# Kernel optimization log

Measured on AMD Instinct MI355X. Metric: run time of the kernel, lower is better.

The kernel has to match this reference:

```python
import jax, jax.numpy as jnp
import numpy as np

H, D, K, FF = 8, 512, 64, 64  # n_head, feature_dim, key_feature_dim, dim_feedforward
L, B = 512, 32
LN_EPS = 1e-5


def _l2norm(x, eps=1e-12):
    # torch F.normalize: x / max(||x||, eps)
    n = jnp.sqrt(jnp.sum(x * x, axis=-1, keepdims=True))
    return x / jnp.maximum(n, eps)


def _layernorm(x, g, b, eps=LN_EPS):
    m = jnp.mean(x, axis=-1, keepdims=True)
    v = jnp.mean((x - m) ** 2, axis=-1, keepdims=True)
    return (x - m) * jax.lax.rsqrt(v + eps) * g + b


def setup_inputs() -> dict:
    key0 = jax.random.key(0)
    ks = jax.random.split(key0, 13)
    n = jax.random.normal
    s_kq = float(np.sqrt(2.0 / K))
    s_v = float(np.sqrt(2.0 / D))
    return {
        "query": n(ks[0], (L, B, D), jnp.float32),
        "key": n(ks[1], (L, B, D), jnp.float32),
        "value": n(ks[2], (L, B, D), jnp.float32),
        "WK": n(ks[3], (H, K, D), jnp.float32) * s_kq,
        "WQ": n(ks[4], (H, K, D), jnp.float32) * s_kq,
        "WV": n(ks[5], (H, D, D), jnp.float32) * s_v,
        "Wt": n(ks[6], (H, D, D), jnp.float32) * 0.04,  # trans_conv (default kaiming-ish scale)
        "W1": n(ks[7], (H, FF, D), jnp.float32) * 0.04,
        "b1": jnp.zeros((H, FF), jnp.float32),
        "W2": n(ks[8], (H, D, FF), jnp.float32) * 0.1,
        "b2": jnp.zeros((H, D), jnp.float32),
        "ln_g": jnp.ones((H, D), jnp.float32),
        "ln_b": jnp.zeros((H, D), jnp.float32),
    }


def reference(query, key, value, WK, WQ, WV, Wt, W1, b1, W2, b2, ln_g, ln_b):
    # query/key/value: [L, B, D]; per-head weights stacked on leading H axis.
    Lq, Bb, Dd = query.shape
    Hh = WK.shape[0]

    # per-head cosine-normalized Q/K projections: [H, B, L, K]
    wq = _l2norm(jnp.einsum('lbd,hkd->hblk', query, WQ))
    wk = _l2norm(jnp.einsum('lbd,hkd->hblk', key, WK))

    # attention scores [H, B, Lq, Lk], temp = 1
    dot = jnp.einsum('hbqc,hbkc->hbqk', wq, wk)
    aff = jax.nn.softmax(dot, axis=-1)
    # custom renorm: divide by column sums over the QUERY axis
    aff = aff / (1e-9 + jnp.sum(aff, axis=2, keepdims=True))

    wv = jnp.einsum('lbd,hed->hble', value, WV)        # [H, B, Lk, D]
    out = jnp.einsum('hbqk,hbke->hbqe', aff, wv)       # [H, B, Lq, D]
    out = jnp.transpose(out, (0, 2, 1, 3))             # [H, L, B, D]

    # residual-style trans_conv(query - out) -> relu
    o = jax.nn.relu(jnp.einsum('hlbd,hed->hlbe', query[None] - out, Wt))

    # TransNonlinear FFN (dropout = identity at eval)
    hff = jax.nn.relu(jnp.einsum('hlbd,hfd->hlbf', o, W1) + b1[:, None, None, :])
    s2 = jnp.einsum('hlbf,hdf->hlbd', hff, W2) + b2[:, None, None, :]
    x = _layernorm(o + s2, ln_g[:, None, None, :], ln_b[:, None, None, :])

    # concat heads on last dim, head 0 first: [L, B, H*D]
    return jnp.transpose(x, (1, 2, 0, 3)).reshape(Lq, Bb, Hh * Dd)
```

## Files before the change

### kernel.cpp

```cpp
#include <hip/hip_runtime.h>
#include <stdint.h>

#define HH 8
#define DDIM 512
#define KHEAD 64
#define FFD 64
#define LLEN 512
#define BBATCH 32
#define NTOK 16384

typedef unsigned short u16;
typedef __attribute__((ext_vector_type(8))) __bf16 bf16x8;
typedef __attribute__((ext_vector_type(4))) float f32x4;

__device__ __forceinline__ float bf2f(u16 u) {
    union { uint32_t i; float f; } v; v.i = ((uint32_t)u) << 16; return v.f;
}
__device__ __forceinline__ u16 f2bf(float f) {
    union { uint32_t i; float f; } v; v.f = f;
    return (u16)((v.i + 0x7FFFu + ((v.i >> 16) & 1u)) >> 16);
}

__device__ __forceinline__ void gload16(const void* g, void* l) {
    __builtin_amdgcn_global_load_lds(
        (const __attribute__((address_space(1))) void*)g,
        (__attribute__((address_space(3))) void*)l, 16, 0, 0);
}

__global__ __launch_bounds__(256) void f2bf4(const float* __restrict__ in,
                                             u16* __restrict__ out, int n4) {
    int i = blockIdx.x * 256 + threadIdx.x;
    if (i >= n4) return;
    float4 v = ((const float4*)in)[i];
    ushort4 o; o.x = f2bf(v.x); o.y = f2bf(v.y); o.z = f2bf(v.z); o.w = f2bf(v.w);
    ((ushort4*)out)[i] = o;
}

enum { M_PLAIN = 0, M_WQK = 1, M_SUBAUX = 2, M_RELU = 3, M_ADDAUX = 4, M_SCALECOL = 5 };

template<int BM, int BN, int MODE>
__global__ __launch_bounds__(256) void mgemm(
    const u16* __restrict__ A, const u16* __restrict__ B, u16* __restrict__ C,
    int Kd, int lda, int ldb, int ldc,
    long Ash, long Asb, long Bsh, long Bsb, long Csh, long Csb, int nB2,
    const float* __restrict__ bias, int biasN,
    const void* __restrict__ auxp, long auxsh, long auxsb, int auxld)
{
    constexpr int WC = (BN == 128) ? 2 : 1;
    constexpr int WR = 4 / WC;
    constexpr int WTM = BM / WR;
    constexpr int WTN = BN / WC;
    constexpr int MF = WTM / 16;
    constexpr int NF = WTN / 16;
    constexpr int NCA = (BM * 64) / 4096;
    constexpr int NCB = (BN * 64) / 4096;
    __shared__ u16 As[BM * 32];
    __shared__ u16 Bs[BN * 32];

    const int z = blockIdx.z;
    const int h2 = z / nB2, b2 = z % nB2;
    const u16* Ab = A + h2 * Ash + b2 * Asb;
    const u16* Bb = B + h2 * Bsh + b2 * Bsb;
    const int m0 = blockIdx.x * BM, n0 = blockIdx.y * BN;
    const int t = threadIdx.x;
    const int lane = t & 63;
    const int w = t >> 6;
    const int wr = w / WC, wc = w % WC;
    const int tb = t * 16;
    const int wb = (t & 192) * 16;

    f32x4 acc[MF][NF];
    #pragma unroll
    for (int m = 0; m < MF; ++m)
        #pragma unroll
        for (int n = 0; n < NF; ++n)
            #pragma unroll
            for (int i = 0; i < 4; ++i) acc[m][n][i] = 0.f;

    const int ko = (lane >> 4) * 16;

    for (int k0 = 0; k0 < Kd; k0 += 32) {
        #pragma unroll
        for (int c = 0; c < NCA; ++c) {
            const int byte = c * 4096 + tb;
            const int row = byte >> 6;
            gload16((const char*)(Ab + (long)(m0 + row) * lda + k0) + (byte & 63),
                    (char*)As + c * 4096 + wb);
        }
        #pragma unroll
        for (int c = 0; c < NCB; ++c) {
            const int byte = c * 4096 + tb;
            const int row = byte >> 6;
            gload16((const char*)(Bb + (long)(n0 + row) * ldb + k0) + (byte & 63),
                    (char*)Bs + c * 4096 + wb);
        }
        __syncthreads();
        bf16x8 af[MF], bfr[NF];
        #pragma unroll
        for (int m = 0; m < MF; ++m)
            af[m] = *(const bf16x8*)((const char*)As + (wr * WTM + m * 16 + (lane & 15)) * 64 + ko);
        #pragma unroll
        for (int n = 0; n < NF; ++n)
            bfr[n] = *(const bf16x8*)((const char*)Bs + (wc * WTN + n * 16 + (lane & 15)) * 64 + ko);
        #pragma unroll
        for (int m = 0; m < MF; ++m)
            #pragma unroll
            for (int n = 0; n < NF; ++n)
                acc[m][n] = __builtin_amdgcn_mfma_f32_16x16x32_bf16(af[m], bfr[n], acc[m][n], 0, 0, 0);
        __syncthreads();
    }

    const int lr = (lane >> 4) * 4;
    const int lc = lane & 15;

    if constexpr (MODE == M_WQK) {
        const int h = (n0 + wc * WTN) >> 6;
        #pragma unroll
        for (int m = 0; m < MF; ++m) {
            #pragma unroll
            for (int i = 0; i < 4; ++i) {
                float s = 0.f;
                #pragma unroll
                for (int n = 0; n < NF; ++n) { const float v = acc[m][n][i]; s += v * v; }
                s += __shfl_xor(s, 1); s += __shfl_xor(s, 2);
                s += __shfl_xor(s, 4); s += __shfl_xor(s, 8);
                const float inv = 1.0f / fmaxf(sqrtf(s), 1e-12f);
                const int r = m0 + wr * WTM + m * 16 + lr + i;
                const int l = r >> 5, bq = r & 31;
                const int sw = (l & 7) << 3;
                u16* rowp = C + (((long)(h * BBATCH + bq) * LLEN + l) * KHEAD);
                #pragma unroll
                for (int n = 0; n < NF; ++n)
                    rowp[(lc + n * 16) ^ sw] = f2bf(acc[m][n][i] * inv);
            }
        }
    } else {
        const long cof = h2 * Csh + b2 * Csb;
        #pragma unroll
        for (int m = 0; m < MF; ++m) {
            #pragma unroll
            for (int i = 0; i < 4; ++i) {
                const int r = m0 + wr * WTM + m * 16 + lr + i;
                #pragma unroll
                for (int n = 0; n < NF; ++n) {
                    const int c = n0 + wc * WTN + n * 16 + lc;
                    float v = acc[m][n][i];
                    if (MODE == M_SUBAUX) {
                        const float* q = (const float*)auxp;
                        v = q[auxsh * h2 + auxsb * b2 + (long)r * auxld + c] - v;
                    } else if (MODE == M_RELU) {
                        if (bias) v += bias[h2 * biasN + c];
                        v = fmaxf(v, 0.0f);
                    } else if (MODE == M_ADDAUX) {
                        v += bias[h2 * biasN + c];
                        const u16* ax = (const u16*)auxp;
                        v += bf2f(ax[auxsh * h2 + auxsb * b2 + (long)r * auxld + c]);
                    } else if (MODE == M_SCALECOL) {
                        const float* cs = (const float*)auxp + auxsh * h2 + auxsb * b2;
                        v *= 1.0f / (1e-9f + cs[c]);
                    }
                    C[cof + (long)r * ldc + c] = f2bf(v);
                }
            }
        }
    }
}

__global__ __launch_bounds__(256) void attn_mfma(
    const u16* __restrict__ wq, const u16* __restrict__ wk,
    u16* __restrict__ P, float* __restrict__ colsum)
{
    __shared__ u16 qs[64 * 64];
    __shared__ u16 ks[512 * 64];
    __shared__ float smax[4][64];
    __shared__ float ssum[4][64];

    const int qt = blockIdx.x, b = blockIdx.y, h = blockIdx.z;
    const long hb = h * BBATCH + b;
    const int t = threadIdx.x;
    const int lane = t & 63, w = t >> 6;
    const int wb = (t & 192) * 16;

    const char* qg = (const char*)(wq + (hb * LLEN + qt * 64) * KHEAD);
    const char* kg = (const char*)(wk + hb * LLEN * KHEAD);
    #pragma unroll
    for (int c = 0; c < 2; ++c)
        gload16(qg + c * 4096 + t * 16, (char*)qs + c * 4096 + wb);
    #pragma unroll
    for (int c = 0; c < 16; ++c)
        gload16(kg + c * 4096 + t * 16, (char*)ks + c * 4096 + wb);
    __syncthreads();

    const int l15 = lane & 15;
    const int g = lane >> 4;
    const int swz = (lane & 7) << 4;

    f32x4 acc[4][8];
    #pragma unroll
    for (int m = 0; m < 4; ++m)
        #pragma unroll
        for (int n = 0; n < 8; ++n)
            #pragma unroll
            for (int i = 0; i < 4; ++i) acc[m][n][i] = 0.f;

    #pragma unroll
    for (int kk = 0; kk < 2; ++kk) {
        bf16x8 af[4];
        #pragma unroll
        for (int m = 0; m < 4; ++m) {
            const int row = m * 16 + l15;
            af[m] = *(const bf16x8*)((const char*)qs + row * 128 + ((g * 16 + kk * 64) ^ swz));
        }
        #pragma unroll
        for (int n = 0; n < 8; ++n) {
            const int row = (w * 8 + n) * 16 + l15;
            const bf16x8 bfr = *(const bf16x8*)((const char*)ks + row * 128 + ((g * 16 + kk * 64) ^ swz));
            #pragma unroll
            for (int m = 0; m < 4; ++m)
                acc[m][n] = __builtin_amdgcn_mfma_f32_16x16x32_bf16(af[m], bfr, acc[m][n], 0, 0, 0);
        }
    }

    float rmax[4][4];
    #pragma unroll
    for (int m = 0; m < 4; ++m)
        #pragma unroll
        for (int i = 0; i < 4; ++i) {
            float mx = acc[m][0][i];
            #pragma unroll
            for (int n = 1; n < 8; ++n) mx = fmaxf(mx, acc[m][n][i]);
            mx = fmaxf(mx, __shfl_xor(mx, 1));
            mx = fmaxf(mx, __shfl_xor(mx, 2));
            mx = fmaxf(mx, __shfl_xor(mx, 4));
            mx = fmaxf(mx, __shfl_xor(mx, 8));
            if (l15 == 0) smax[w][m * 16 + g * 4 + i] = mx;
        }
    __syncthreads();
    #pragma unroll
    for (int m = 0; m < 4; ++m)
        #pragma unroll
        for (int i = 0; i < 4; ++i) {
            const int r = m * 16 + g * 4 + i;
            rmax[m][i] = fmaxf(fmaxf(smax[0][r], smax[1][r]),
                               fmaxf(smax[2][r], smax[3][r]));
        }
    float rinv[4][4];
    #pragma unroll
    for (int m = 0; m < 4; ++m)
        #pragma unroll
        for (int i = 0; i < 4; ++i) {
            float s = 0.f;
            #pragma unroll
            for (int n = 0; n < 8; ++n) {
                acc[m][n][i] = __expf(acc[m][n][i] - rmax[m][i]);
                s += acc[m][n][i];
            }
            s += __shfl_xor(s, 1); s += __shfl_xor(s, 2);
            s += __shfl_xor(s, 4); s += __shfl_xor(s, 8);
            if (l15 == 0) ssum[w][m * 16 + g * 4 + i] = s;
        }
    __syncthreads();
    #pragma unroll
    for (int m = 0; m < 4; ++m)
        #pragma unroll
        for (int i = 0; i < 4; ++i) {
            const int r = m * 16 + g * 4 + i;
            rinv[m][i] = 1.0f / (ssum[0][r] + ssum[1][r] + ssum[2][r] + ssum[3][r]);
        }

    u16* Pb = P + (hb * LLEN + qt * 64) * LLEN + w * 128;
    float cs[8];
    #pragma unroll
    for (int n = 0; n < 8; ++n) cs[n] = 0.f;
    #pragma unroll
    for (int m = 0; m < 4; ++m)
        #pragma unroll
        for (int i = 0; i < 4; ++i) {
            const int r = m * 16 + g * 4 + i;
            u16* pr = Pb + (long)r * LLEN + l15;
            const float iv = rinv[m][i];
            #pragma unroll
            for (int n = 0; n < 8; ++n) {
                const float p = acc[m][n][i] * iv;
                pr[n * 16] = f2bf(p);
                cs[n] += p;
            }
        }
    #pragma unroll
    for (int n = 0; n < 8; ++n) {
        cs[n] += __shfl_xor(cs[n], 16);
        cs[n] += __shfl_xor(cs[n], 32);
    }
    if (lane < 16) {
        float* cb = colsum + hb * 512 + w * 128 + lane;
        #pragma unroll
        for (int n = 0; n < 8; ++n) atomicAdd(&cb[n * 16], cs[n]);
    }
}

__global__ __launch_bounds__(256) void ln_out(
    const u16* __restrict__ x, const float* __restrict__ g,
    const float* __restrict__ bb, float* __restrict__ out)
{
    const int t = threadIdx.x;
    const int w = t >> 6, lane = t & 63;
    const long row = (long)blockIdx.x * 4 + w;
    const int h = (int)(row >> 14);
    const int t2 = (int)(row & 16383);
    const int b = t2 >> 9, l = t2 & 511;
    const u16* xp = x + row * DDIM;
    float v[8];
    float s = 0.f, sq = 0.f;
    #pragma unroll
    for (int j = 0; j < 8; ++j) {
        v[j] = bf2f(xp[j * 64 + lane]);
        s += v[j]; sq += v[j] * v[j];
    }
    #pragma unroll
    for (int off = 32; off >= 1; off >>= 1) {
        s += __shfl_xor(s, off);
        sq += __shfl_xor(sq, off);
    }
    const float mean = s * (1.0f / 512.0f);
    const float var = sq * (1.0f / 512.0f) - mean * mean;
    const float rs = rsqrtf(var + 1e-5f);
    const float* gp = g + h * DDIM;
    const float* bp = bb + h * DDIM;
    float* op = out + ((long)l * BBATCH + b) * (HH * DDIM) + h * DDIM;
    #pragma unroll
    for (int j = 0; j < 8; ++j) {
        const int d = j * 64 + lane;
        op[d] = (v[j] - mean) * rs * gp[d] + bp[d];
    }
}

extern "C" void kernel_launch(void* const* d_in, const int* in_sizes, int n_in,
                              void* d_out, int out_size, void* d_ws, size_t ws_size,
                              hipStream_t stream) {
    const float* query = (const float*)d_in[0];
    const float* key   = (const float*)d_in[1];
    const float* value = (const float*)d_in[2];
    const float* WK = (const float*)d_in[3];
    const float* WQ = (const float*)d_in[4];
    const float* WV = (const float*)d_in[5];
    const float* Wt = (const float*)d_in[6];
    const float* W1 = (const float*)d_in[7];
    const float* b1 = (const float*)d_in[8];
    const float* W2 = (const float*)d_in[9];
    const float* b2 = (const float*)d_in[10];
    const float* lng = (const float*)d_in[11];
    const float* lnb = (const float*)d_in[12];

    char* ws = (char*)d_ws;
    u16* qbf  = (u16*)(ws);
    u16* kbf  = (u16*)(ws + 16777216);
    u16* WQbf = (u16*)(ws + 33554432);
    u16* WKbf = (u16*)(ws + 34078720);
    u16* P    = (u16*)(ws);
    u16* preLN = P;
    u16* vbf  = (u16*)(ws + 134217728);
    u16* WVbf = (u16*)(ws + 150994944);
    u16* o    = (u16*)(ws + 134217728);
    float* colsum = (float*)(ws + 268435456);
    u16* hff  = (u16*)(ws + 268959744);
    u16* wq   = (u16*)(ws + 285736960);
    u16* wk   = (u16*)(ws + 302514176);
    u16* Wtbf = (u16*)(ws + 285736960);
    u16* W1bf = (u16*)(ws + 289931264);
    u16* W2bf = (u16*)(ws + 290455552);
    u16* qmo = (u16*)d_out;
    u16* wvT = (u16*)((char*)d_out + 134217728);

    if (ws_size < 319291392u) return;

    hipMemsetAsync(colsum, 0, 524288, stream);
    const dim3 blk(256);

    f2bf4<<<dim3(8192), blk, 0, stream>>>(query, qbf, 2097152);
    f2bf4<<<dim3(8192), blk, 0, stream>>>(key,   kbf, 2097152);
    f2bf4<<<dim3(8192), blk, 0, stream>>>(value, vbf, 2097152);
    f2bf4<<<dim3(256),  blk, 0, stream>>>(WQ, WQbf, 65536);
    f2bf4<<<dim3(256),  blk, 0, stream>>>(WK, WKbf, 65536);
    f2bf4<<<dim3(2048), blk, 0, stream>>>(WV, WVbf, 524288);

    mgemm<128, 128, M_WQK><<<dim3(128, 4, 1), blk, 0, stream>>>(
        qbf, WQbf, wq, 512, 512, 512, 0,
        0, 0, 0, 0, 0, 0, 1, nullptr, 0, nullptr, 0, 0, 0);
    mgemm<128, 128, M_WQK><<<dim3(128, 4, 1), blk, 0, stream>>>(
        kbf, WKbf, wk, 512, 512, 512, 0,
        0, 0, 0, 0, 0, 0, 1, nullptr, 0, nullptr, 0, 0, 0);

    attn_mfma<<<dim3(8, 32, 8), blk, 0, stream>>>(wq, wk, P, colsum);

    f2bf4<<<dim3(2048), blk, 0, stream>>>(Wt, Wtbf, 524288);
    f2bf4<<<dim3(256),  blk, 0, stream>>>(W1, W1bf, 65536);
    f2bf4<<<dim3(256),  blk, 0, stream>>>(W2, W2bf, 65536);

    mgemm<128, 128, M_SCALECOL><<<dim3(4, 4, 256), blk, 0, stream>>>(
        WVbf, vbf, wvT, 512, 512, BBATCH * DDIM, 512,
        (long)DDIM * DDIM, 0, 0, DDIM,
        (long)BBATCH * DDIM * LLEN, (long)DDIM * LLEN, 32,
        nullptr, 0, colsum, (long)BBATCH * 512, 512, 0);

    mgemm<128, 128, M_SUBAUX><<<dim3(4, 4, 256), blk, 0, stream>>>(
        P, wvT, qmo, 512, 512, 512, 512,
        (long)BBATCH * LLEN * LLEN, (long)LLEN * LLEN,
        (long)BBATCH * DDIM * LLEN, (long)DDIM * LLEN,
        (long)BBATCH * LLEN * DDIM, (long)LLEN * DDIM, 32,
        nullptr, 0, query, 0, DDIM, BBATCH * DDIM);

    mgemm<128, 128, M_RELU><<<dim3(128, 4, 8), blk, 0, stream>>>(
        qmo, Wtbf, o, 512, 512, 512, 512,
        (long)NTOK * DDIM, 0, (long)DDIM * DDIM, 0,
        (long)NTOK * DDIM, 0, 1, nullptr, 512, nullptr, 0, 0, 0);

    mgemm<128, 64, M_RELU><<<dim3(128, 1, 8), blk, 0, stream>>>(
        o, W1bf, hff, 512, 512, 512, 64,
        (long)NTOK * DDIM, 0, (long)FFD * DDIM, 0,
        (long)NTOK * FFD, 0, 1, b1, 64, nullptr, 0, 0, 0);

    mgemm<128, 128, M_ADDAUX><<<dim3(128, 4, 8), blk, 0, stream>>>(
        hff, W2bf, preLN, 64, 64, 64, 512,
        (long)NTOK * FFD, 0, (long)DDIM * FFD, 0,
        (long)NTOK * DDIM, 0, 1, b2, 512, o, (long)NTOK * DDIM, 0, 512);

    ln_out<<<dim3(32768), blk, 0, stream>>>(preLN, lng, lnb, (float*)d_out);
}
```

Measured before the change: 812.3 us.

## Fuse FFN GEMMs into one kernel, reorder batched grid, read bf16 query

The two FFN GEMMs (o·W1 with ReLU, then hff·W2 plus bias and residual) become a single kernel. The hidden activations stay in shared memory, and W2 is pre-swizzled on conversion to avoid LDS bank conflicts. This removes the global round trip of the hff tensor and one launch. The batched GEMMs also get new block-z to head/batch mappings so that concurrently running blocks share operands in cache. The subtract epilogue now reads the bf16 copy of query instead of fp32, trading a little precision for fewer bytes read.

```diff
diff --git a/kernel.cpp b/kernel.cpp
--- a/kernel.cpp
+++ b/kernel.cpp
@@ -36,9 +36,25 @@
     ((ushort4*)out)[i] = o;
 }
 
+__global__ __launch_bounds__(256) void f2bf_w2(const float* __restrict__ in,
+                                               u16* __restrict__ out) {
+    const int id = blockIdx.x * 256 + threadIdx.x;
+    const int r = id >> 3, cg = (id & 7) * 8;
+    const float* ip = in + r * 64 + cg;
+    const int sw = (r & 7) << 3;
+    float4 a = ((const float4*)ip)[0];
+    float4 b = ((const float4*)ip)[1];
+    ushort4 lo, hi;
+    lo.x = f2bf(a.x); lo.y = f2bf(a.y); lo.z = f2bf(a.z); lo.w = f2bf(a.w);
+    hi.x = f2bf(b.x); hi.y = f2bf(b.y); hi.z = f2bf(b.z); hi.w = f2bf(b.w);
+    u16* op = out + r * 64 + (cg ^ sw);
+    ((ushort4*)op)[0] = lo;
+    ((ushort4*)op)[1] = hi;
+}
+
 enum { M_PLAIN = 0, M_WQK = 1, M_SUBAUX = 2, M_RELU = 3, M_ADDAUX = 4, M_SCALECOL = 5 };
 
-template<int BM, int BN, int MODE>
+template<int BM, int BN, int MODE, int ZMAP>
 __global__ __launch_bounds__(256) void mgemm(
     const u16* __restrict__ A, const u16* __restrict__ B, u16* __restrict__ C,
     int Kd, int lda, int ldb, int ldc,
@@ -58,7 +74,10 @@
     __shared__ u16 Bs[BN * 32];
 
     const int z = blockIdx.z;
-    const int h2 = z / nB2, b2 = z % nB2;
+    int h2, b2;
+    if (ZMAP == 0)      { h2 = z / nB2;      b2 = z % nB2; }
+    else if (ZMAP == 1) { h2 = z & 7;        b2 = z >> 3; }
+    else                { h2 = (z >> 3) & 7; b2 = ((z >> 6) << 3) | (z & 7); }
     const u16* Ab = A + h2 * Ash + b2 * Asb;
     const u16* Bb = B + h2 * Bsh + b2 * Bsb;
     const int m0 = blockIdx.x * BM, n0 = blockIdx.y * BN;
@@ -146,8 +165,8 @@
                     const int c = n0 + wc * WTN + n * 16 + lc;
                     float v = acc[m][n][i];
                     if (MODE == M_SUBAUX) {
-                        const float* q = (const float*)auxp;
-                        v = q[auxsh * h2 + auxsb * b2 + (long)r * auxld + c] - v;
+                        const u16* q = (const u16*)auxp;
+                        v = bf2f(q[auxsh * h2 + auxsb * b2 + (long)r * auxld + c]) - v;
                     } else if (MODE == M_RELU) {
                         if (bias) v += bias[h2 * biasN + c];
                         v = fmaxf(v, 0.0f);
@@ -295,6 +314,127 @@
         float* cb = colsum + hb * 512 + w * 128 + lane;
         #pragma unroll
         for (int n = 0; n < 8; ++n) atomicAdd(&cb[n * 16], cs[n]);
+    }
+}
+
+__global__ __launch_bounds__(256) void ffn_fused(
+    const u16* __restrict__ o, const u16* __restrict__ W1,
+    const float* __restrict__ b1, const u16* __restrict__ W2sw,
+    const float* __restrict__ b2, u16* __restrict__ preLN)
+{
+    __shared__ u16 As[128 * 32];
+    __shared__ u16 B1s[64 * 32];
+    __shared__ u16 hffs[128 * 64];
+    __shared__ u16 W2c[128 * 64];
+
+    const int h = blockIdx.z;
+    const int m0 = blockIdx.x * 128;
+    const int t = threadIdx.x;
+    const int lane = t & 63, w = t >> 6;
+    const int l15 = lane & 15, g = lane >> 4;
+    const int wb = (t & 192) * 16;
+    const u16* ob = o + ((long)h * NTOK + m0) * DDIM;
+    const u16* w1b = W1 + h * (FFD * DDIM);
+
+    f32x4 acc[2][4];
+    #pragma unroll
+    for (int m = 0; m < 2; ++m)
+        #pragma unroll
+        for (int n = 0; n < 4; ++n)
+            #pragma unroll
+            for (int i = 0; i < 4; ++i) acc[m][n][i] = 0.f;
+
+    for (int k0 = 0; k0 < 512; k0 += 32) {
+        #pragma unroll
+        for (int c = 0; c < 2; ++c) {
+            const int byte = c * 4096 + t * 16;
+            const int row = byte >> 6;
+            gload16((const char*)(ob + (long)row * DDIM + k0) + (byte & 63),
+                    (char*)As + c * 4096 + wb);
+        }
+        {
+            const int byte = t * 16;
+            const int row = byte >> 6;
+            gload16((const char*)(w1b + (long)row * DDIM + k0) + (byte & 63),
+                    (char*)B1s + wb);
+        }
+        __syncthreads();
+        bf16x8 af[2], bfr[4];
+        #pragma unroll
+        for (int m = 0; m < 2; ++m)
+            af[m] = *(const bf16x8*)((const char*)As + (w * 32 + m * 16 + l15) * 64 + g * 16);
+        #pragma unroll
+        for (int n = 0; n < 4; ++n)
+            bfr[n] = *(const bf16x8*)((const char*)B1s + (n * 16 + l15) * 64 + g * 16);
+        #pragma unroll
+        for (int m = 0; m < 2; ++m)
+            #pragma unroll
+            for (int n = 0; n < 4; ++n)
+                acc[m][n] = __builtin_amdgcn_mfma_f32_16x16x32_bf16(af[m], bfr[n], acc[m][n], 0, 0, 0);
+        __syncthreads();
+    }
+    #pragma unroll
+    for (int m = 0; m < 2; ++m)
+        #pragma unroll
+        for (int i = 0; i < 4; ++i) {
+            const int row = w * 32 + m * 16 + g * 4 + i;
+            const int sw = (row & 7) << 3;
+            #pragma unroll
+            for (int n = 0; n < 4; ++n) {
+                const int col = n * 16 + l15;
+                const float v = fmaxf(acc[m][n][i] + b1[h * FFD + col], 0.0f);
+                hffs[row * 64 + (col ^ sw)] = f2bf(v);
+            }
+        }
+
+    for (int cc = 0; cc < 4; ++cc) {
+        __syncthreads();
+        #pragma unroll
+        for (int c = 0; c < 4; ++c) {
+            const int byte = c * 4096 + t * 16;
+            gload16((const char*)(W2sw + h * 32768) + cc * 16384 + byte,
+                    (char*)W2c + c * 4096 + wb);
+        }
+        __syncthreads();
+        f32x4 acc2[2][8];
+        #pragma unroll
+        for (int m = 0; m < 2; ++m)
+            #pragma unroll
+            for (int n = 0; n < 8; ++n)
+                #pragma unroll
+                for (int i = 0; i < 4; ++i) acc2[m][n][i] = 0.f;
+        #pragma unroll
+        for (int kk = 0; kk < 2; ++kk) {
+            bf16x8 paf[2];
+            #pragma unroll
+            for (int m = 0; m < 2; ++m) {
+                const int row = w * 32 + m * 16 + l15;
+                paf[m] = *(const bf16x8*)((const char*)hffs + row * 128 +
+                                          (((kk * 4 + g) ^ (row & 7)) * 16));
+            }
+            #pragma unroll
+            for (int n = 0; n < 8; ++n) {
+                const int row = n * 16 + l15;
+                const bf16x8 bfr = *(const bf16x8*)((const char*)W2c + row * 128 +
+                                                    (((kk * 4 + g) ^ (row & 7)) * 16));
+                #pragma unroll
+                for (int m = 0; m < 2; ++m)
+                    acc2[m][n] = __builtin_amdgcn_mfma_f32_16x16x32_bf16(paf[m], bfr, acc2[m][n], 0, 0, 0);
+            }
+        }
+        #pragma unroll
+        for (int m = 0; m < 2; ++m)
+            #pragma unroll
+            for (int i = 0; i < 4; ++i) {
+                const int row = w * 32 + m * 16 + g * 4 + i;
+                #pragma unroll
+                for (int n = 0; n < 8; ++n) {
+                    const int col = cc * 128 + n * 16 + l15;
+                    float v = acc2[m][n][i] + b2[h * DDIM + col] +
+                              bf2f(ob[(long)row * DDIM + col]);
+                    preLN[((long)h * NTOK + m0 + row) * DDIM + col] = f2bf(v);
+                }
+            }
     }
 }
 
@@ -352,17 +492,16 @@
     const float* lnb = (const float*)d_in[12];
 
     char* ws = (char*)d_ws;
-    u16* qbf  = (u16*)(ws);
-    u16* kbf  = (u16*)(ws + 16777216);
-    u16* WQbf = (u16*)(ws + 33554432);
-    u16* WKbf = (u16*)(ws + 34078720);
+    u16* kbf  = (u16*)(ws);
+    u16* WQbf = (u16*)(ws + 16777216);
+    u16* WKbf = (u16*)(ws + 17301504);
     u16* P    = (u16*)(ws);
     u16* preLN = P;
     u16* vbf  = (u16*)(ws + 134217728);
     u16* WVbf = (u16*)(ws + 150994944);
     u16* o    = (u16*)(ws + 134217728);
     float* colsum = (float*)(ws + 268435456);
-    u16* hff  = (u16*)(ws + 268959744);
+    u16* qbf  = (u16*)(ws + 268959744);
     u16* wq   = (u16*)(ws + 285736960);
     u16* wk   = (u16*)(ws + 302514176);
     u16* Wtbf = (u16*)(ws + 285736960);
@@ -383,10 +522,10 @@
     f2bf4<<<dim3(256),  blk, 0, stream>>>(WK, WKbf, 65536);
     f2bf4<<<dim3(2048), blk, 0, stream>>>(WV, WVbf, 524288);
 
-    mgemm<128, 128, M_WQK><<<dim3(128, 4, 1), blk, 0, stream>>>(
+    mgemm<128, 128, M_WQK, 0><<<dim3(128, 4, 1), blk, 0, stream>>>(
         qbf, WQbf, wq, 512, 512, 512, 0,
         0, 0, 0, 0, 0, 0, 1, nullptr, 0, nullptr, 0, 0, 0);
-    mgemm<128, 128, M_WQK><<<dim3(128, 4, 1), blk, 0, stream>>>(
+    mgemm<128, 128, M_WQK, 0><<<dim3(128, 4, 1), blk, 0, stream>>>(
         kbf, WKbf, wk, 512, 512, 512, 0,
         0, 0, 0, 0, 0, 0, 1, nullptr, 0, nullptr, 0, 0, 0);
 
@@ -394,35 +533,27 @@
 
     f2bf4<<<dim3(2048), blk, 0, stream>>>(Wt, Wtbf, 524288);
     f2bf4<<<dim3(256),  blk, 0, stream>>>(W1, W1bf, 65536);
-    f2bf4<<<dim3(256),  blk, 0, stream>>>(W2, W2bf, 65536);
-
-    mgemm<128, 128, M_SCALECOL><<<dim3(4, 4, 256), blk, 0, stream>>>(
+    f2bf_w2<<<dim3(128), blk, 0, stream>>>(W2, W2bf);
+
+    mgemm<128, 128, M_SCALECOL, 2><<<dim3(4, 4, 256), blk, 0, stream>>>(
         WVbf, vbf, wvT, 512, 512, BBATCH * DDIM, 512,
         (long)DDIM * DDIM, 0, 0, DDIM,
         (long)BBATCH * DDIM * LLEN, (long)DDIM * LLEN, 32,
         nullptr, 0, colsum, (long)BBATCH * 512, 512, 0);
 
-    mgemm<128, 128, M_SUBAUX><<<dim3(4, 4, 256), blk, 0, stream>>>(
+    mgemm<128, 128, M_SUBAUX, 1><<<dim3(4, 4, 256), blk, 0, stream>>>(
         P, wvT, qmo, 512, 512, 512, 512,
         (long)BBATCH * LLEN * LLEN, (long)LLEN * LLEN,
         (long)BBATCH * DDIM * LLEN, (long)DDIM * LLEN,
         (long)BBATCH * LLEN * DDIM, (long)LLEN * DDIM, 32,
-        nullptr, 0, query, 0, DDIM, BBATCH * DDIM);
-
-    mgemm<128, 128, M_RELU><<<dim3(128, 4, 8), blk, 0, stream>>>(
+        nullptr, 0, qbf, 0, DDIM, BBATCH * DDIM);
+
+    mgemm<128, 128, M_RELU, 0><<<dim3(128, 4, 8), blk, 0, stream>>>(
         qmo, Wtbf, o, 512, 512, 512, 512,
         (long)NTOK * DDIM, 0, (long)DDIM * DDIM, 0,
         (long)NTOK * DDIM, 0, 1, nullptr, 512, nullptr, 0, 0, 0);
 
-    mgemm<128, 64, M_RELU><<<dim3(128, 1, 8), blk, 0, stream>>>(
-        o, W1bf, hff, 512, 512, 512, 64,
-        (long)NTOK * DDIM, 0, (long)FFD * DDIM, 0,
-        (long)NTOK * FFD, 0, 1, b1, 64, nullptr, 0, 0, 0);
-
-    mgemm<128, 128, M_ADDAUX><<<dim3(128, 4, 8), blk, 0, stream>>>(
-        hff, W2bf, preLN, 64, 64, 64, 512,
-        (long)NTOK * FFD, 0, (long)DDIM * FFD, 0,
-        (long)NTOK * DDIM, 0, 1, b2, 512, o, (long)NTOK * DDIM, 0, 512);
+    ffn_fused<<<dim3(128, 1, 8), blk, 0, stream>>>(o, W1bf, b1, W2bf, b2, preLN);
 
     ln_out<<<dim3(32768), blk, 0, stream>>>(preLN, lng, lnb, (float*)d_out);
 }
```

Result: slower. 935.5 us (+15.2%).
